# Performance work log

Measured on AMD Instinct MI355X. Metric: run time of the kernel, lower is better.

## Reference

```python
import jax, jax.numpy as jnp
import numpy as np

N = 6144      # nodes
DIN = 65      # input_dim (1 time + 64 space coords)
DOUT = 65     # output_dim per head
H = 4         # nheads
EPS = 1e-7
MIN = 1e-15
# curvature c = 1 throughout (MultiHeadGraphAttentionLayer hardcodes curvature=1)

def arcosh(z):
    return jnp.log(z + jnp.sqrt(jnp.maximum(z * z - 1.0, 0.0)))

def hyp_proj(u):
    # project onto hyperboloid: recompute time coord
    y = u[..., 1:]
    t = jnp.sqrt(1.0 + jnp.sum(y * y, -1, keepdims=True))
    return jnp.concatenate([t, y], -1)

def expmap0(u):
    v = u[..., 1:]
    n = jnp.maximum(jnp.linalg.norm(v, axis=-1, keepdims=True), MIN)
    return jnp.concatenate([jnp.cosh(n), jnp.sinh(n) * v / n], -1)

def logmap0(x):
    y = x[..., 1:]
    n = jnp.maximum(jnp.linalg.norm(y, axis=-1, keepdims=True), MIN)
    t = jnp.maximum(x[..., :1], 1.0 + EPS)
    return jnp.concatenate([jnp.zeros_like(t), arcosh(t) * y / n], -1)

def hyp_linear(x, W):
    # HypLinear (use_bias=False, eval mode): mobius_matvec = exp0(log0(x) @ W^T), then proj
    return hyp_proj(expmap0(logmap0(x) @ W.T))

def to_poincare(x):
    return x[..., 1:] / (x[..., :1] + 1.0)

def to_hyperboloid(p):
    s = jnp.sum(p * p, -1, keepdims=True)
    return jnp.concatenate([1.0 + s, 2.0 * p], -1) / jnp.maximum(1.0 - s, MIN)

def mobius_half(v):
    # 0.5 (x) v  (mobius scalar multiplication, c=1)
    n = jnp.maximum(jnp.linalg.norm(v, axis=-1, keepdims=True), MIN)
    return jnp.tanh(0.5 * jnp.arctanh(jnp.minimum(n, 1.0 - EPS))) * v / n

def head(x, adj_t, Wa, Wd, Wo):
    att = hyp_linear(x, Wa)   # [N, DOUT]
    red = hyp_linear(x, Wd)   # [N, DOUT]
    # pairwise hyperboloid sqdist via Minkowski inner product (negate time coord)
    am = att.at[:, 0].multiply(-1.0)
    theta = jnp.maximum(-(am @ att.T), 1.0 + EPS)          # [N, N]
    S = jnp.minimum(arcosh(theta) ** 2, 50.0)
    # coef[i, j] = -adj[j, i] * sqdist for incoming edges (mask = adj^T)
    coef = jnp.where(adj_t > 0.01, -adj_t * S, 0.0)
    # F.normalize along incoming-edge axis (zeros don't change the L2 norm)
    a = coef / jnp.maximum(jnp.linalg.norm(coef, axis=-1, keepdims=True), 1e-12)
    pv = to_poincare(red)                                   # [N, DOUT-1]
    lam = 2.0 / jnp.maximum(1.0 - jnp.sum(pv * pv, -1), MIN)  # conformal factors [N]
    num = (a * lam[None, :]) @ pv                           # [N, DOUT-1]
    den = jnp.sum(jnp.abs(a) * (lam - 1.0)[None, :], -1, keepdims=True)
    m = mobius_half(num / jnp.maximum(den, MIN))            # mobius midpoint
    return hyp_linear(to_hyperboloid(m), Wo)                # [N, DOUT]

def reference(x, adj, W_att, W_data, W_out, W_lin):
    adj_t = adj.T
    hs = jnp.stack([head(x, adj_t, W_att[h], W_data[h], W_out[h]) for h in range(H)], axis=1)  # [N, H, DOUT]
    p = to_poincare(hs).reshape(x.shape[0], -1)             # PoincareBall.concat -> [N, H*(DOUT-1)]
    return hyp_linear(to_hyperboloid(p), W_lin)             # [N, H*DOUT]

def setup_inputs():
    key = jax.random.key(0)
    ks = jax.random.split(key, 8)
    sp = 0.1 * jax.random.normal(ks[0], (N, DIN - 1), jnp.float32)
    x = jnp.concatenate([jnp.sqrt(1.0 + jnp.sum(sp * sp, -1, keepdims=True)), sp], -1)
    adj = (jax.random.uniform(ks[1], (N, N)) < 32.0 / N).astype(jnp.float32)
    adj = jnp.maximum(adj, jnp.eye(N, dtype=jnp.float32))  # every node >=1 incoming edge
    def xavier(k, shape):
        b = (6.0 / (shape[0] + shape[1])) ** 0.5
        return jax.random.uniform(k, shape, jnp.float32, -b, b)
    W_att = jnp.stack([xavier(jax.random.fold_in(ks[2], h), (DOUT, DIN)) for h in range(H)])
    W_data = jnp.stack([xavier(jax.random.fold_in(ks[3], h), (DOUT, DIN)) for h in range(H)])
    W_out = jnp.stack([xavier(jax.random.fold_in(ks[4], h), (DOUT, DOUT)) for h in range(H)])
    W_lin = xavier(ks[5], (H * DOUT, H * (DOUT - 1) + 1))
    return {"x": x, "adj": adj, "W_att": W_att, "W_data": W_data, "W_out": W_out, "W_lin": W_lin}
```

## Files before the change

kernel.cpp:

```cpp
#include <hip/hip_runtime.h>
#include <math.h>

#define N 6144
#define H 4
#define CAP 128
#define MINF 1e-15f
#define ONE_EPS  1.0000001192092896f
#define ONE_MEPS 0.9999998807907104f

__device__ __forceinline__ float wave_reduce_sum(float v) {
    v += __shfl_xor(v, 32, 64);
    v += __shfl_xor(v, 16, 64);
    v += __shfl_xor(v, 8, 64);
    v += __shfl_xor(v, 4, 64);
    v += __shfl_xor(v, 2, 64);
    v += __shfl_xor(v, 1, 64);
    return v;
}

__device__ __forceinline__ float arcosh_f(float z) {
    return logf(z + sqrtf(fmaxf(z * z - 1.0f, 0.0f)));
}

__global__ void k_prep(const float* __restrict__ x, float* __restrict__ lmv,
                       const float* __restrict__ W_att, const float* __restrict__ W_data,
                       const float* __restrict__ W_out,
                       float* __restrict__ Bp, float* __restrict__ Bo,
                       int* __restrict__ cnt) {
    int b = blockIdx.x;
    if (b < 1536) {
        int i = b * 4 + (threadIdx.x >> 6);
        int lane = threadIdx.x & 63;
        float y = x[i * 65 + 1 + lane];
        float ss = wave_reduce_sum(y * y);
        float n = fmaxf(sqrtf(ss), MINF);
        float t = fmaxf(x[i * 65], ONE_EPS);
        lmv[i * 64 + lane] = arcosh_f(t) * y / n;
    } else if (b < 1728) {
        int tid = (b - 1536) * 256 + threadIdx.x;
        int m = tid >> 12;
        int r = tid & 4095;
        int k = r >> 6, o = r & 63;
        const float* src;
        if (m < 4) src = W_att + m * 65 * 65;
        else if (m < 8) src = W_data + (m - 4) * 65 * 65;
        else src = W_out + (m - 8) * 65 * 65;
        float val = src[(1 + o) * 65 + (1 + k)];
        if (m < 8) Bp[m * 4096 + k * 64 + o] = val;
        else Bo[(m - 8) * 4096 + k * 64 + o] = val;
    } else {
        cnt[(b - 1728) * 256 + threadIdx.x] = 0;
    }
}

__global__ void __launch_bounds__(256) k_csr_gemm(
        const float* __restrict__ adj, int* __restrict__ cnt, int* __restrict__ idx,
        const float* __restrict__ lmv, const float* __restrict__ Bp,
        float* __restrict__ attv, float2* __restrict__ a0l, float* __restrict__ pv) {
    __shared__ float As[16][64];
    __shared__ float Bs[16][64];
    __shared__ float Cs[64][65];
    if (blockIdx.x < 768) {
        int my = blockIdx.x / 96;
        int ix = blockIdx.x % 96;
        const float* Bb = Bp + (size_t)my * 4096;
        int i0 = ix * 64;
        int tid = threadIdx.x;
        int tx = tid & 15, ty = tid >> 4;
        float acc[4][4] = {};
        for (int k0 = 0; k0 < 64; k0 += 16) {
            {
                int mm = tid >> 2, kq = tid & 3;
                float4 v = *(const float4*)(lmv + (size_t)(i0 + mm) * 64 + k0 + kq * 4);
                As[kq * 4 + 0][mm] = v.x;
                As[kq * 4 + 1][mm] = v.y;
                As[kq * 4 + 2][mm] = v.z;
                As[kq * 4 + 3][mm] = v.w;
            }
            {
                int kk = tid >> 4, o4 = tid & 15;
                float4 bvv = *(const float4*)(Bb + (k0 + kk) * 64 + o4 * 4);
                *(float4*)&Bs[kk][o4 * 4] = bvv;
            }
            __syncthreads();
            #pragma unroll
            for (int kk = 0; kk < 16; kk++) {
                float4 av = *(const float4*)&As[kk][ty * 4];
                float4 bv = *(const float4*)&Bs[kk][tx * 4];
                float a[4] = {av.x, av.y, av.z, av.w};
                float b[4] = {bv.x, bv.y, bv.z, bv.w};
                #pragma unroll
                for (int r = 0; r < 4; r++)
                    #pragma unroll
                    for (int c = 0; c < 4; c++) acc[r][c] += a[r] * b[c];
            }
            __syncthreads();
        }
        #pragma unroll
        for (int r = 0; r < 4; r++)
            #pragma unroll
            for (int c = 0; c < 4; c++)
                Cs[ty * 4 + r][tx * 4 + c] = acc[r][c];
        __syncthreads();
        int w = tid >> 6, lane = tid & 63;
        int h = my & 3;
        bool isAtt = my < 4;
        #pragma unroll 1
        for (int r16 = 0; r16 < 16; r16++) {
            int row = w * 16 + r16;
            int i = i0 + row;
            float u = Cs[row][lane];
            float nn = fmaxf(sqrtf(wave_reduce_sum(u * u)), MINF);
            if (isAtt) {
                float sha = sinhf(nn);
                attv[((size_t)h * N + i) * 64 + lane] = sha * u / nn;
                if (lane == 0) a0l[h * N + i].x = coshf(nn);
            } else {
                float shd = sinhf(nn), chd = coshf(nn);
                float pvd = (shd * u / nn) / (chd + 1.0f);
                pv[((size_t)h * N + i) * 64 + lane] = pvd;
                float sp = wave_reduce_sum(pvd * pvd);
                if (lane == 0) a0l[h * N + i].y = 2.0f / fmaxf(1.0f - sp, MINF);
            }
        }
    } else {
        const unsigned total4 = (unsigned)N * N / 4;
        const float4* a4 = (const float4*)adj;
        for (unsigned e = (blockIdx.x - 768) * 256 + threadIdx.x; e < total4;
             e += 4096u * 256u) {
            float4 v = a4[e];
            unsigned base = e * 4u;
            float vals[4] = {v.x, v.y, v.z, v.w};
            #pragma unroll
            for (int q = 0; q < 4; q++) {
                if (vals[q] > 0.01f) {
                    unsigned t = base + q;
                    int j = t / N;
                    int i = t % N;
                    int pos = atomicAdd(&cnt[i], 1);
                    if (pos < CAP) idx[i * CAP + pos] = j;
                }
            }
        }
    }
}

__global__ void __launch_bounds__(256) k_attn(
        const int* __restrict__ cnt, const int* __restrict__ idx,
        const float* __restrict__ attv, const float2* __restrict__ a0l,
        const float* __restrict__ pv, float* __restrict__ lm2) {
    __shared__ float wls[4][CAP];
    __shared__ int jls[4][CAP];
    int w = threadIdx.x >> 6, lane = threadIdx.x & 63;
    int i = blockIdx.x * 4 + w;
    int h = blockIdx.y;
    const float* attvh = attv + (size_t)h * N * 64;
    const float* pvh = pv + (size_t)h * N * 64;
    const float2* a0lh = a0l + (size_t)h * N;

    int c = lane & 3;
    float4 aireg[4];
    #pragma unroll
    for (int q = 0; q < 4; q++)
        aireg[q] = *(const float4*)(attvh + (size_t)i * 64 + q * 16 + c * 4);
    float ai0 = a0lh[i].x;
    int nn = min(cnt[i], CAP);

    float accd = 0.f, accss = 0.f;
    for (int base = 0; base < nn; base += 16) {
        int t = base + (lane >> 2);
        bool act = t < nn;
        int j = act ? idx[i * CAP + t] : i;
        float2 al = a0lh[j];
        float d = 0.f;
        #pragma unroll
        for (int q = 0; q < 4; q++) {
            float4 b = *(const float4*)(attvh + (size_t)j * 64 + q * 16 + c * 4);
            float4 a = aireg[q];
            d += a.x * b.x + a.y * b.y + a.z * b.z + a.w * b.w;
        }
        d += __shfl_xor(d, 1, 64);
        d += __shfl_xor(d, 2, 64);
        float theta = fmaxf(ai0 * al.x - d, ONE_EPS);
        float ar = arcosh_f(theta);
        float S = fminf(ar * ar, 50.0f);
        if (!act) S = 0.f;
        if (c == 0) {
            accd += S * (al.y - 1.0f);
            accss += S * S;
            wls[w][t] = S * al.y;
            jls[w][t] = j;
        }
    }
    accd = wave_reduce_sum(accd);
    accss = wave_reduce_sum(accss);
    float nrm = fmaxf(sqrtf(accss), 1e-12f);
    float den = fmaxf(accd / nrm, MINF);
    float scl = 1.0f / (nrm * den);

    float accn = 0.f;
    #pragma unroll 4
    for (int t = 0; t < nn; t++) {
        int j = jls[w][t];
        float wq = wls[w][t];
        accn = fmaf(wq, pvh[(size_t)j * 64 + lane], accn);
    }
    float v = -scl * accn;
    float nv = fmaxf(sqrtf(wave_reduce_sum(v * v)), MINF);
    float nc = fminf(nv, ONE_MEPS);
    float mh = tanhf(0.5f * atanhf(nc));
    float md = mh * v / nv;
    float s = wave_reduce_sum(md * md);
    float Dh = fmaxf(1.0f - s, MINF);
    float hb0 = (1.0f + s) / Dh;
    float hbv = 2.0f * md / Dh;
    float nh = fmaxf(2.0f * sqrtf(s) / Dh, MINF);
    float t2 = fmaxf(hb0, ONE_EPS);
    lm2[((size_t)h * N + i) * 64 + lane] = arcosh_f(t2) * hbv / nh;
}

__global__ void __launch_bounds__(256) k_gemm_out(
        const float* __restrict__ lm2, const float* __restrict__ Bo,
        float* __restrict__ p) {
    __shared__ float As[16][64];
    __shared__ float Bs[16][64];
    __shared__ float Cs[64][65];
    int h = blockIdx.y;
    const float* Ab = lm2 + (size_t)h * N * 64;
    const float* Bb = Bo + (size_t)h * 4096;
    int i0 = blockIdx.x * 64;
    int tid = threadIdx.x;
    int tx = tid & 15, ty = tid >> 4;
    float acc[4][4] = {};
    for (int k0 = 0; k0 < 64; k0 += 16) {
        {
            int mm = tid >> 2, kq = tid & 3;
            float4 v = *(const float4*)(Ab + (size_t)(i0 + mm) * 64 + k0 + kq * 4);
            As[kq * 4 + 0][mm] = v.x;
            As[kq * 4 + 1][mm] = v.y;
            As[kq * 4 + 2][mm] = v.z;
            As[kq * 4 + 3][mm] = v.w;
        }
        {
            int kk = tid >> 4, o4 = tid & 15;
            float4 bvv = *(const float4*)(Bb + (k0 + kk) * 64 + o4 * 4);
            *(float4*)&Bs[kk][o4 * 4] = bvv;
        }
        __syncthreads();
        #pragma unroll
        for (int kk = 0; kk < 16; kk++) {
            float4 av = *(const float4*)&As[kk][ty * 4];
            float4 bv = *(const float4*)&Bs[kk][tx * 4];
            float a[4] = {av.x, av.y, av.z, av.w};
            float b[4] = {bv.x, bv.y, bv.z, bv.w};
            #pragma unroll
            for (int r = 0; r < 4; r++)
                #pragma unroll
                for (int c = 0; c < 4; c++) acc[r][c] += a[r] * b[c];
        }
        __syncthreads();
    }
    #pragma unroll
    for (int r = 0; r < 4; r++)
        #pragma unroll
        for (int c = 0; c < 4; c++)
            Cs[ty * 4 + r][tx * 4 + c] = acc[r][c];
    __syncthreads();
    int w = tid >> 6, lane = tid & 63;
    #pragma unroll 1
    for (int r16 = 0; r16 < 16; r16++) {
        int row = w * 16 + r16;
        int i = i0 + row;
        float u = Cs[row][lane];
        float nv = fmaxf(sqrtf(wave_reduce_sum(u * u)), MINF);
        float sh = sinhf(nv), ch = coshf(nv);
        p[(size_t)i * 256 + h * 64 + lane] = (sh * u / nv) / (ch + 1.0f);
    }
}

__global__ void k_final_logmap(const float* __restrict__ p, float* __restrict__ lmF) {
    __shared__ float part[4];
    int i = blockIdx.x;
    int t = threadIdx.x;
    int w = t >> 6;
    float pd = p[(size_t)i * 256 + t];
    float ss = wave_reduce_sum(pd * pd);
    if ((t & 63) == 0) part[w] = ss;
    __syncthreads();
    float s = part[0] + part[1] + part[2] + part[3];
    float Dh = fmaxf(1.0f - s, MINF);
    float hb0 = (1.0f + s) / Dh;
    float hbv = 2.0f * pd / Dh;
    float n = fmaxf(2.0f * sqrtf(s) / Dh, MINF);
    float tt = fmaxf(hb0, ONE_EPS);
    lmF[(size_t)i * 256 + t] = arcosh_f(tt) * hbv / n;
}

__global__ void k_final_gemm(const float* __restrict__ A,
                             const float* __restrict__ Wl,
                             float* __restrict__ U) {
    __shared__ float As[16][64];
    __shared__ float Bs[16][64];
    int i0 = blockIdx.x * 64;
    int o0 = blockIdx.y * 64;
    int tid = threadIdx.x;
    int tx = tid & 15, ty = tid >> 4;
    float acc[4][4] = {};
    for (int k0 = 0; k0 < 256; k0 += 16) {
        {
            int mm = tid >> 2;
            int kq = tid & 3;
            const float4 v = *(const float4*)(A + (size_t)(i0 + mm) * 256 + k0 + kq * 4);
            As[kq * 4 + 0][mm] = v.x;
            As[kq * 4 + 1][mm] = v.y;
            As[kq * 4 + 2][mm] = v.z;
            As[kq * 4 + 3][mm] = v.w;
        }
        {
            int oo = tid >> 2;
            int kq = tid & 3;
            int o = o0 + oo;
            if (o < 259) {
                const float* src = Wl + (size_t)(1 + o) * 257 + 1 + k0 + kq * 4;
                Bs[kq * 4 + 0][oo] = src[0];
                Bs[kq * 4 + 1][oo] = src[1];
                Bs[kq * 4 + 2][oo] = src[2];
                Bs[kq * 4 + 3][oo] = src[3];
            } else {
                Bs[kq * 4 + 0][oo] = 0.f;
                Bs[kq * 4 + 1][oo] = 0.f;
                Bs[kq * 4 + 2][oo] = 0.f;
                Bs[kq * 4 + 3][oo] = 0.f;
            }
        }
        __syncthreads();
        #pragma unroll
        for (int kk = 0; kk < 16; kk++) {
            float4 av = *(const float4*)&As[kk][ty * 4];
            float4 bv = *(const float4*)&Bs[kk][tx * 4];
            float a[4] = {av.x, av.y, av.z, av.w};
            float b[4] = {bv.x, bv.y, bv.z, bv.w};
            #pragma unroll
            for (int r = 0; r < 4; r++)
                #pragma unroll
                for (int c = 0; c < 4; c++) acc[r][c] += a[r] * b[c];
        }
        __syncthreads();
    }
    #pragma unroll
    for (int r = 0; r < 4; r++) {
        int i = i0 + ty * 4 + r;
        #pragma unroll
        for (int c = 0; c < 4; c++) {
            int o = o0 + tx * 4 + c;
            if (o < 259) U[(size_t)i * 260 + o] = acc[r][c];
        }
    }
}

__global__ void k_final_epilogue(const float* __restrict__ U, float* __restrict__ out) {
    __shared__ float part[4];
    int i = blockIdx.x;
    int t = threadIdx.x;
    float a = U[(size_t)i * 260 + t];
    float b = (t < 3) ? U[(size_t)i * 260 + 256 + t] : 0.f;
    float ss = wave_reduce_sum(a * a + b * b);
    if ((t & 63) == 0) part[t >> 6] = ss;
    __syncthreads();
    ss = part[0] + part[1] + part[2] + part[3];
    float nv = fmaxf(sqrtf(ss), MINF);
    float sh = sinhf(nv);
    float scale = sh / nv;
    out[(size_t)i * 260 + 1 + t] = scale * a;
    if (t < 3) out[(size_t)i * 260 + 257 + t] = scale * b;
    if (t == 0) out[(size_t)i * 260] = sqrtf(1.0f + sh * sh);
}

extern "C" void kernel_launch(void* const* d_in, const int* in_sizes, int n_in,
                              void* d_out, int out_size, void* d_ws, size_t ws_size,
                              hipStream_t stream) {
    const float* x = (const float*)d_in[0];
    const float* adj = (const float*)d_in[1];
    const float* W_att = (const float*)d_in[2];
    const float* W_data = (const float*)d_in[3];
    const float* W_out = (const float*)d_in[4];
    const float* W_lin = (const float*)d_in[5];
    float* out = (float*)d_out;

    char* ws = (char*)d_ws;
    size_t off = 0;
    auto alloc = [&](size_t bytes) {
        void* ptr = ws + off;
        off += (bytes + 255) & ~(size_t)255;
        return ptr;
    };
    int* cnt = (int*)alloc((size_t)N * 4);
    int* idx = (int*)alloc((size_t)N * CAP * 4);
    float* lmv = (float*)alloc((size_t)N * 64 * 4);
    float* attv = (float*)alloc((size_t)H * N * 64 * 4);
    float2* a0l = (float2*)alloc((size_t)H * N * 8);
    float* pvb = (float*)alloc((size_t)H * N * 64 * 4);
    float* lm2 = (float*)alloc((size_t)H * N * 64 * 4);
    float* U = (float*)alloc((size_t)N * 260 * 4);
    float* Bp = (float*)alloc((size_t)8 * 4096 * 4);
    float* Bo = (float*)alloc((size_t)4 * 4096 * 4);
    float* lmF = attv;
    float* p = pvb;

    k_prep<<<1752, 256, 0, stream>>>(x, lmv, W_att, W_data, W_out, Bp, Bo, cnt);
    k_csr_gemm<<<4864, 256, 0, stream>>>(adj, cnt, idx, lmv, Bp, attv, a0l, pvb);
    k_attn<<<dim3(N / 4, H), 256, 0, stream>>>(cnt, idx, attv, a0l, pvb, lm2);
    k_gemm_out<<<dim3(N / 64, H), 256, 0, stream>>>(lm2, Bo, p);
    k_final_logmap<<<N, 256, 0, stream>>>(p, lmF);
    k_final_gemm<<<dim3(N / 64, 5), 256, 0, stream>>>(lmF, W_lin, U);
    k_final_epilogue<<<N, 256, 0, stream>>>(U, out);
}
```

Measured before the change: 349.2 us.

## Fuse prep into CSR/GEMM and merge output-stage kernels into two fused kernels

Removes the separate prep kernel: the first linear's log-map scaling and weight transposition are now done inside the GEMM tile loads, and the counter zeroing becomes a memset. The output GEMM, log-map and final GEMM and epilogue are merged into two kernels that keep per-row intermediates in shared memory, cutting the launch count from seven to four plus a memset and removing the U and p round-trips. The tradeoffs are smaller tiles with lower arithmetic intensity in the final GEMM (8 rows per block, reloading W_lin per block) and strided uncoalesced weight and x loads.

```diff
diff --git a/kernel.cpp b/kernel.cpp
--- a/kernel.cpp
+++ b/kernel.cpp
@@ -22,65 +22,52 @@
     return logf(z + sqrtf(fmaxf(z * z - 1.0f, 0.0f)));
 }
 
-__global__ void k_prep(const float* __restrict__ x, float* __restrict__ lmv,
-                       const float* __restrict__ W_att, const float* __restrict__ W_data,
-                       const float* __restrict__ W_out,
-                       float* __restrict__ Bp, float* __restrict__ Bo,
-                       int* __restrict__ cnt) {
-    int b = blockIdx.x;
-    if (b < 1536) {
-        int i = b * 4 + (threadIdx.x >> 6);
-        int lane = threadIdx.x & 63;
-        float y = x[i * 65 + 1 + lane];
-        float ss = wave_reduce_sum(y * y);
-        float n = fmaxf(sqrtf(ss), MINF);
-        float t = fmaxf(x[i * 65], ONE_EPS);
-        lmv[i * 64 + lane] = arcosh_f(t) * y / n;
-    } else if (b < 1728) {
-        int tid = (b - 1536) * 256 + threadIdx.x;
-        int m = tid >> 12;
-        int r = tid & 4095;
-        int k = r >> 6, o = r & 63;
-        const float* src;
-        if (m < 4) src = W_att + m * 65 * 65;
-        else if (m < 8) src = W_data + (m - 4) * 65 * 65;
-        else src = W_out + (m - 8) * 65 * 65;
-        float val = src[(1 + o) * 65 + (1 + k)];
-        if (m < 8) Bp[m * 4096 + k * 64 + o] = val;
-        else Bo[(m - 8) * 4096 + k * 64 + o] = val;
-    } else {
-        cnt[(b - 1728) * 256 + threadIdx.x] = 0;
-    }
-}
-
 __global__ void __launch_bounds__(256) k_csr_gemm(
         const float* __restrict__ adj, int* __restrict__ cnt, int* __restrict__ idx,
-        const float* __restrict__ lmv, const float* __restrict__ Bp,
+        const float* __restrict__ x,
+        const float* __restrict__ W_att, const float* __restrict__ W_data,
         float* __restrict__ attv, float2* __restrict__ a0l, float* __restrict__ pv) {
+    __shared__ float scale[64];
     __shared__ float As[16][64];
     __shared__ float Bs[16][64];
     __shared__ float Cs[64][65];
     if (blockIdx.x < 768) {
         int my = blockIdx.x / 96;
         int ix = blockIdx.x % 96;
-        const float* Bb = Bp + (size_t)my * 4096;
         int i0 = ix * 64;
+        const float* W = (my < 4) ? (W_att + (size_t)my * 4225)
+                                  : (W_data + (size_t)(my - 4) * 4225);
         int tid = threadIdx.x;
+        int w = tid >> 6, lane = tid & 63;
+        for (int r = 0; r < 16; r++) {
+            int row = w * 16 + r;
+            int i = i0 + row;
+            float val = x[i * 65 + 1 + lane];
+            float ss = wave_reduce_sum(val * val);
+            if (lane == 0)
+                scale[row] = arcosh_f(fmaxf(x[i * 65], ONE_EPS)) /
+                             fmaxf(sqrtf(ss), MINF);
+        }
+        __syncthreads();
         int tx = tid & 15, ty = tid >> 4;
         float acc[4][4] = {};
         for (int k0 = 0; k0 < 64; k0 += 16) {
             {
                 int mm = tid >> 2, kq = tid & 3;
-                float4 v = *(const float4*)(lmv + (size_t)(i0 + mm) * 64 + k0 + kq * 4);
-                As[kq * 4 + 0][mm] = v.x;
-                As[kq * 4 + 1][mm] = v.y;
-                As[kq * 4 + 2][mm] = v.z;
-                As[kq * 4 + 3][mm] = v.w;
-            }
-            {
-                int kk = tid >> 4, o4 = tid & 15;
-                float4 bvv = *(const float4*)(Bb + (k0 + kk) * 64 + o4 * 4);
-                *(float4*)&Bs[kk][o4 * 4] = bvv;
+                float sc = scale[mm];
+                const float* xr = x + (size_t)(i0 + mm) * 65 + 1 + k0 + kq * 4;
+                As[kq * 4 + 0][mm] = sc * xr[0];
+                As[kq * 4 + 1][mm] = sc * xr[1];
+                As[kq * 4 + 2][mm] = sc * xr[2];
+                As[kq * 4 + 3][mm] = sc * xr[3];
+            }
+            {
+                int o = tid & 63, kb = (tid >> 6) * 4;
+                const float* wr = W + (size_t)(1 + o) * 65 + 1 + k0 + kb;
+                Bs[kb + 0][o] = wr[0];
+                Bs[kb + 1][o] = wr[1];
+                Bs[kb + 2][o] = wr[2];
+                Bs[kb + 3][o] = wr[3];
             }
             __syncthreads();
             #pragma unroll
@@ -102,12 +89,11 @@
             for (int c = 0; c < 4; c++)
                 Cs[ty * 4 + r][tx * 4 + c] = acc[r][c];
         __syncthreads();
-        int w = tid >> 6, lane = tid & 63;
+        bool isAtt = my < 4;
         int h = my & 3;
-        bool isAtt = my < 4;
         #pragma unroll 1
-        for (int r16 = 0; r16 < 16; r16++) {
-            int row = w * 16 + r16;
+        for (int r = 0; r < 16; r++) {
+            int row = w * 16 + r;
             int i = i0 + row;
             float u = Cs[row][lane];
             float nn = fmaxf(sqrtf(wave_reduce_sum(u * u)), MINF);
@@ -219,161 +205,154 @@
     lm2[((size_t)h * N + i) * 64 + lane] = arcosh_f(t2) * hbv / nh;
 }
 
-__global__ void __launch_bounds__(256) k_gemm_out(
-        const float* __restrict__ lm2, const float* __restrict__ Bo,
-        float* __restrict__ p) {
-    __shared__ float As[16][64];
+__global__ void __launch_bounds__(256) k_out_fused(
+        const float* __restrict__ lm2, const float* __restrict__ W_out,
+        float* __restrict__ lmF) {
+    __shared__ float As[16][32];
     __shared__ float Bs[16][64];
-    __shared__ float Cs[64][65];
-    int h = blockIdx.y;
-    const float* Ab = lm2 + (size_t)h * N * 64;
-    const float* Bb = Bo + (size_t)h * 4096;
-    int i0 = blockIdx.x * 64;
+    __shared__ float Ps[32][260];
+    int i0 = blockIdx.x * 32;
     int tid = threadIdx.x;
     int tx = tid & 15, ty = tid >> 4;
-    float acc[4][4] = {};
-    for (int k0 = 0; k0 < 64; k0 += 16) {
-        {
-            int mm = tid >> 2, kq = tid & 3;
-            float4 v = *(const float4*)(Ab + (size_t)(i0 + mm) * 64 + k0 + kq * 4);
-            As[kq * 4 + 0][mm] = v.x;
-            As[kq * 4 + 1][mm] = v.y;
-            As[kq * 4 + 2][mm] = v.z;
-            As[kq * 4 + 3][mm] = v.w;
-        }
-        {
-            int kk = tid >> 4, o4 = tid & 15;
-            float4 bvv = *(const float4*)(Bb + (k0 + kk) * 64 + o4 * 4);
-            *(float4*)&Bs[kk][o4 * 4] = bvv;
-        }
+    for (int h = 0; h < H; h++) {
+        const float* Ab = lm2 + (size_t)h * N * 64;
+        const float* W = W_out + (size_t)h * 4225;
+        float acc[2][4] = {};
+        for (int k0 = 0; k0 < 64; k0 += 16) {
+            {
+                int mm = tid & 31, kb = (tid >> 5) * 2;
+                As[kb + 0][mm] = Ab[(size_t)(i0 + mm) * 64 + k0 + kb + 0];
+                As[kb + 1][mm] = Ab[(size_t)(i0 + mm) * 64 + k0 + kb + 1];
+            }
+            {
+                int o = tid & 63, kb = (tid >> 6) * 4;
+                const float* wr = W + (size_t)(1 + o) * 65 + 1 + k0 + kb;
+                Bs[kb + 0][o] = wr[0];
+                Bs[kb + 1][o] = wr[1];
+                Bs[kb + 2][o] = wr[2];
+                Bs[kb + 3][o] = wr[3];
+            }
+            __syncthreads();
+            #pragma unroll
+            for (int kk = 0; kk < 16; kk++) {
+                float4 bv = *(const float4*)&Bs[kk][tx * 4];
+                float a0 = As[kk][ty * 2 + 0];
+                float a1 = As[kk][ty * 2 + 1];
+                acc[0][0] += a0 * bv.x; acc[0][1] += a0 * bv.y;
+                acc[0][2] += a0 * bv.z; acc[0][3] += a0 * bv.w;
+                acc[1][0] += a1 * bv.x; acc[1][1] += a1 * bv.y;
+                acc[1][2] += a1 * bv.z; acc[1][3] += a1 * bv.w;
+            }
+            __syncthreads();
+        }
+        #pragma unroll
+        for (int r = 0; r < 2; r++)
+            #pragma unroll
+            for (int c2 = 0; c2 < 4; c2++)
+                Ps[ty * 2 + r][h * 64 + tx * 4 + c2] = acc[r][c2];
         __syncthreads();
-        #pragma unroll
-        for (int kk = 0; kk < 16; kk++) {
-            float4 av = *(const float4*)&As[kk][ty * 4];
-            float4 bv = *(const float4*)&Bs[kk][tx * 4];
-            float a[4] = {av.x, av.y, av.z, av.w};
-            float b[4] = {bv.x, bv.y, bv.z, bv.w};
-            #pragma unroll
-            for (int r = 0; r < 4; r++)
-                #pragma unroll
-                for (int c = 0; c < 4; c++) acc[r][c] += a[r] * b[c];
-        }
-        __syncthreads();
-    }
-    #pragma unroll
-    for (int r = 0; r < 4; r++)
-        #pragma unroll
-        for (int c = 0; c < 4; c++)
-            Cs[ty * 4 + r][tx * 4 + c] = acc[r][c];
+    }
+    int w = tid >> 6, lane = tid & 63;
+    #pragma unroll 1
+    for (int r = 0; r < 8; r++) {
+        int row = w * 8 + r;
+        int i = i0 + row;
+        float pr[4];
+        float sp[4];
+        #pragma unroll
+        for (int h = 0; h < 4; h++) {
+            float u = Ps[row][h * 64 + lane];
+            float nv = fmaxf(sqrtf(wave_reduce_sum(u * u)), MINF);
+            float sh = sinhf(nv), ch = coshf(nv);
+            float pd = (sh * u / nv) / (ch + 1.0f);
+            pr[h] = pd;
+            sp[h] = wave_reduce_sum(pd * pd);
+        }
+        float s = ((sp[0] + sp[1]) + sp[2]) + sp[3];
+        float Dh = fmaxf(1.0f - s, MINF);
+        float hb0 = (1.0f + s) / Dh;
+        float nrm = fmaxf(2.0f * sqrtf(s) / Dh, MINF);
+        float tt = fmaxf(hb0, ONE_EPS);
+        float fac = arcosh_f(tt);
+        #pragma unroll
+        for (int h = 0; h < 4; h++) {
+            float hbv = 2.0f * pr[h] / Dh;
+            lmF[(size_t)i * 256 + h * 64 + lane] = fac * hbv / nrm;
+        }
+    }
+}
+
+__global__ void __launch_bounds__(256) k_final_fused(
+        const float* __restrict__ lmF, const float* __restrict__ Wl,
+        float* __restrict__ out) {
+    __shared__ float Af[8][260];
+    __shared__ float Bs[16][64];
+    __shared__ float Ls[8][260];
+    int i0 = blockIdx.x * 8;
+    int tid = threadIdx.x;
+    {
+        int r = tid >> 5, c4 = (tid & 31) * 8;
+        const float* src = lmF + (size_t)(i0 + r) * 256 + c4;
+        float4 v0 = *(const float4*)(src);
+        float4 v1 = *(const float4*)(src + 4);
+        *(float4*)&Af[r][c4] = v0;
+        *(float4*)&Af[r][c4 + 4] = v1;
+    }
+    int col = tid & 63, rg = tid >> 6;
+    for (int co = 0; co < 5; co++) {
+        int o0 = co * 64;
+        float acc0 = 0.f, acc1 = 0.f;
+        for (int k0 = 0; k0 < 256; k0 += 16) {
+            {
+                int o = tid & 63, kb = (tid >> 6) * 4;
+                int oc = o0 + o;
+                if (oc < 259) {
+                    const float* wr = Wl + (size_t)(1 + oc) * 257 + 1 + k0 + kb;
+                    Bs[kb + 0][o] = wr[0];
+                    Bs[kb + 1][o] = wr[1];
+                    Bs[kb + 2][o] = wr[2];
+                    Bs[kb + 3][o] = wr[3];
+                } else {
+                    Bs[kb + 0][o] = 0.f; Bs[kb + 1][o] = 0.f;
+                    Bs[kb + 2][o] = 0.f; Bs[kb + 3][o] = 0.f;
+                }
+            }
+            __syncthreads();
+            #pragma unroll
+            for (int kk = 0; kk < 16; kk++) {
+                float b = Bs[kk][col];
+                acc0 += Af[rg * 2 + 0][k0 + kk] * b;
+                acc1 += Af[rg * 2 + 1][k0 + kk] * b;
+            }
+            __syncthreads();
+        }
+        if (o0 + col < 260) {
+            Ls[rg * 2 + 0][o0 + col] = acc0;
+            Ls[rg * 2 + 1][o0 + col] = acc1;
+        }
+    }
     __syncthreads();
     int w = tid >> 6, lane = tid & 63;
     #pragma unroll 1
-    for (int r16 = 0; r16 < 16; r16++) {
-        int row = w * 16 + r16;
+    for (int r = 0; r < 2; r++) {
+        int row = w * 2 + r;
         int i = i0 + row;
-        float u = Cs[row][lane];
-        float nv = fmaxf(sqrtf(wave_reduce_sum(u * u)), MINF);
-        float sh = sinhf(nv), ch = coshf(nv);
-        p[(size_t)i * 256 + h * 64 + lane] = (sh * u / nv) / (ch + 1.0f);
-    }
-}
-
-__global__ void k_final_logmap(const float* __restrict__ p, float* __restrict__ lmF) {
-    __shared__ float part[4];
-    int i = blockIdx.x;
-    int t = threadIdx.x;
-    int w = t >> 6;
-    float pd = p[(size_t)i * 256 + t];
-    float ss = wave_reduce_sum(pd * pd);
-    if ((t & 63) == 0) part[w] = ss;
-    __syncthreads();
-    float s = part[0] + part[1] + part[2] + part[3];
-    float Dh = fmaxf(1.0f - s, MINF);
-    float hb0 = (1.0f + s) / Dh;
-    float hbv = 2.0f * pd / Dh;
-    float n = fmaxf(2.0f * sqrtf(s) / Dh, MINF);
-    float tt = fmaxf(hb0, ONE_EPS);
-    lmF[(size_t)i * 256 + t] = arcosh_f(tt) * hbv / n;
-}
-
-__global__ void k_final_gemm(const float* __restrict__ A,
-                             const float* __restrict__ Wl,
-                             float* __restrict__ U) {
-    __shared__ float As[16][64];
-    __shared__ float Bs[16][64];
-    int i0 = blockIdx.x * 64;
-    int o0 = blockIdx.y * 64;
-    int tid = threadIdx.x;
-    int tx = tid & 15, ty = tid >> 4;
-    float acc[4][4] = {};
-    for (int k0 = 0; k0 < 256; k0 += 16) {
-        {
-            int mm = tid >> 2;
-            int kq = tid & 3;
-            const float4 v = *(const float4*)(A + (size_t)(i0 + mm) * 256 + k0 + kq * 4);
-            As[kq * 4 + 0][mm] = v.x;
-            As[kq * 4 + 1][mm] = v.y;
-            As[kq * 4 + 2][mm] = v.z;
-            As[kq * 4 + 3][mm] = v.w;
-        }
-        {
-            int oo = tid >> 2;
-            int kq = tid & 3;
-            int o = o0 + oo;
-            if (o < 259) {
-                const float* src = Wl + (size_t)(1 + o) * 257 + 1 + k0 + kq * 4;
-                Bs[kq * 4 + 0][oo] = src[0];
-                Bs[kq * 4 + 1][oo] = src[1];
-                Bs[kq * 4 + 2][oo] = src[2];
-                Bs[kq * 4 + 3][oo] = src[3];
-            } else {
-                Bs[kq * 4 + 0][oo] = 0.f;
-                Bs[kq * 4 + 1][oo] = 0.f;
-                Bs[kq * 4 + 2][oo] = 0.f;
-                Bs[kq * 4 + 3][oo] = 0.f;
-            }
-        }
-        __syncthreads();
-        #pragma unroll
-        for (int kk = 0; kk < 16; kk++) {
-            float4 av = *(const float4*)&As[kk][ty * 4];
-            float4 bv = *(const float4*)&Bs[kk][tx * 4];
-            float a[4] = {av.x, av.y, av.z, av.w};
-            float b[4] = {bv.x, bv.y, bv.z, bv.w};
-            #pragma unroll
-            for (int r = 0; r < 4; r++)
-                #pragma unroll
-                for (int c = 0; c < 4; c++) acc[r][c] += a[r] * b[c];
-        }
-        __syncthreads();
-    }
-    #pragma unroll
-    for (int r = 0; r < 4; r++) {
-        int i = i0 + ty * 4 + r;
-        #pragma unroll
-        for (int c = 0; c < 4; c++) {
-            int o = o0 + tx * 4 + c;
-            if (o < 259) U[(size_t)i * 260 + o] = acc[r][c];
-        }
-    }
-}
-
-__global__ void k_final_epilogue(const float* __restrict__ U, float* __restrict__ out) {
-    __shared__ float part[4];
-    int i = blockIdx.x;
-    int t = threadIdx.x;
-    float a = U[(size_t)i * 260 + t];
-    float b = (t < 3) ? U[(size_t)i * 260 + 256 + t] : 0.f;
-    float ss = wave_reduce_sum(a * a + b * b);
-    if ((t & 63) == 0) part[t >> 6] = ss;
-    __syncthreads();
-    ss = part[0] + part[1] + part[2] + part[3];
-    float nv = fmaxf(sqrtf(ss), MINF);
-    float sh = sinhf(nv);
-    float scale = sh / nv;
-    out[(size_t)i * 260 + 1 + t] = scale * a;
-    if (t < 3) out[(size_t)i * 260 + 257 + t] = scale * b;
-    if (t == 0) out[(size_t)i * 260] = sqrtf(1.0f + sh * sh);
+        float u0 = Ls[row][lane];
+        float u1 = Ls[row][64 + lane];
+        float u2 = Ls[row][128 + lane];
+        float u3 = Ls[row][192 + lane];
+        float u4 = (lane < 3) ? Ls[row][256 + lane] : 0.f;
+        float ss = wave_reduce_sum(u0 * u0 + u1 * u1 + u2 * u2 + u3 * u3 + u4 * u4);
+        float nv = fmaxf(sqrtf(ss), MINF);
+        float sh = sinhf(nv);
+        float sc = sh / nv;
+        out[(size_t)i * 260 + 1 + lane]   = sc * u0;
+        out[(size_t)i * 260 + 65 + lane]  = sc * u1;
+        out[(size_t)i * 260 + 129 + lane] = sc * u2;
+        out[(size_t)i * 260 + 193 + lane] = sc * u3;
+        if (lane < 3) out[(size_t)i * 260 + 257 + lane] = sc * u4;
+        if (lane == 0) out[(size_t)i * 260] = sqrtf(1.0f + sh * sh);
+    }
 }
 
 extern "C" void kernel_launch(void* const* d_in, const int* in_sizes, int n_in,
@@ -396,22 +375,16 @@
     };
     int* cnt = (int*)alloc((size_t)N * 4);
     int* idx = (int*)alloc((size_t)N * CAP * 4);
-    float* lmv = (float*)alloc((size_t)N * 64 * 4);
     float* attv = (float*)alloc((size_t)H * N * 64 * 4);
     float2* a0l = (float2*)alloc((size_t)H * N * 8);
     float* pvb = (float*)alloc((size_t)H * N * 64 * 4);
     float* lm2 = (float*)alloc((size_t)H * N * 64 * 4);
-    float* U = (float*)alloc((size_t)N * 260 * 4);
-    float* Bp = (float*)alloc((size_t)8 * 4096 * 4);
-    float* Bo = (float*)alloc((size_t)4 * 4096 * 4);
     float* lmF = attv;
-    float* p = pvb;
-
-    k_prep<<<1752, 256, 0, stream>>>(x, lmv, W_att, W_data, W_out, Bp, Bo, cnt);
-    k_csr_gemm<<<4864, 256, 0, stream>>>(adj, cnt, idx, lmv, Bp, attv, a0l, pvb);
+
+    hipMemsetAsync(cnt, 0, (size_t)N * 4, stream);
+    k_csr_gemm<<<4864, 256, 0, stream>>>(adj, cnt, idx, x, W_att, W_data,
+                                         attv, a0l, pvb);
     k_attn<<<dim3(N / 4, H), 256, 0, stream>>>(cnt, idx, attv, a0l, pvb, lm2);
-    k_gemm_out<<<dim3(N / 64, H), 256, 0, stream>>>(lm2, Bo, p);
-    k_final_logmap<<<N, 256, 0, stream>>>(p, lmF);
-    k_final_gemm<<<dim3(N / 64, 5), 256, 0, stream>>>(lmF, W_lin, U);
-    k_final_epilogue<<<N, 256, 0, stream>>>(U, out);
-}
+    k_out_fused<<<N / 32, 256, 0, stream>>>(lm2, W_out, lmF);
+    k_final_fused<<<N / 8, 256, 0, stream>>>(lmF, W_lin, out);
+}
```

New measurement: 992.7 us. 2.84x slower.
